# Performance work log

Hardware: AMD Instinct MI355X
Metric: run time of the kernel (lower is better)

## Reference

```python
import jax, jax.numpy as jnp
import numpy as np

N, SD, VD, ED, E, NG, NA, NB = 512, 256, 128, 128, 262144, 16, 16, 5


def _lin_init(key, fan_in, fan_out):
    # torch.nn.Linear default: U(-1/sqrt(fan_in), 1/sqrt(fan_in)); stored as (in, out)
    lim = 1.0 / np.sqrt(fan_in)
    return jax.random.uniform(key, (fan_in, fan_out), jnp.float32, -lim, lim)


def setup_inputs() -> dict:
    key = jax.random.key(0)
    ks = jax.random.split(key, 20)
    s = jax.random.normal(ks[0], (N, SD), jnp.float32)
    v = jax.random.normal(ks[1], (N, 3, VD), jnp.float32)
    p = jax.random.normal(ks[2], (N, 3), jnp.float32)
    e = jax.random.normal(ks[3], (E, ED), jnp.float32)
    batch = jnp.sort(jax.random.randint(ks[4], (N,), 0, NG))
    edge_index_global = jax.random.randint(ks[5], (2, E), 0, N)
    W_sm = _lin_init(ks[6], SD, SD); b_sm = jnp.zeros((SD,), jnp.float32)
    W_bm = _lin_init(ks[7], ED, SD); b_bm = jnp.zeros((SD,), jnp.float32)
    W_b0 = _lin_init(ks[8], SD + 1, SD); b_b0 = jnp.zeros((SD,), jnp.float32)
    W_b1 = _lin_init(ks[9], SD, NB); b_b1 = jnp.zeros((NB,), jnp.float32)
    W_c = _lin_init(ks[10], VD, 1)  # no bias
    W_a = _lin_init(ks[11], SD, NA); b_a = jnp.zeros((NA,), jnp.float32)
    return {"s": s, "v": v, "p": p, "e": e, "batch": batch,
            "edge_index_global": edge_index_global,
            "W_sm": W_sm, "b_sm": b_sm, "W_bm": W_bm, "b_bm": b_bm,
            "W_b0": W_b0, "b_b0": b_b0, "W_b1": W_b1, "b_b1": b_b1,
            "W_c": W_c, "W_a": W_a, "b_a": b_a}


def reference(s, v, p, e, batch, edge_index_global,
              W_sm, b_sm, W_bm, b_bm, W_b0, b_b0, W_b1, b_b1, W_c, W_a, b_a):
    # shared_mapping: Linear + SiLU
    s = jax.nn.silu(s @ W_sm + b_sm)                      # [N, SD]
    coords_pred = (v @ W_c)[..., 0]                       # [N, 3]
    atoms_pred = s @ W_a + b_a                            # [N, NA]
    j, i = edge_index_global[0], edge_index_global[1]
    n = s.shape[0]
    # coords_param == 'data': coords = p + pred, then per-graph mean centering
    coords_pred = p + coords_pred
    seg_sum = jax.ops.segment_sum(coords_pred, batch, num_segments=NG)
    counts = jax.ops.segment_sum(jnp.ones((n, 1), coords_pred.dtype), batch, num_segments=NG)
    mean = seg_sum / jnp.maximum(counts, 1.0)
    coords_pred = coords_pred - mean[batch]
    # squared pairwise distance per edge
    d = jnp.sum((coords_pred[i] - coords_pred[j]) ** 2, axis=-1, keepdims=True)  # [E, 1]
    # sparse -> dense -> sparse symmetrization of edge features (as in the source)
    e_dense = jnp.zeros((n, n, e.shape[-1]), e.dtype).at[j, i].set(e)
    e_dense = 0.5 * (e_dense + jnp.transpose(e_dense, (1, 0, 2)))
    e_sym = e_dense[j, i]                                 # [E, ED]
    f = s[i] + s[j] + (e_sym @ W_bm + b_bm)               # [E, SD]
    edge = jnp.concatenate([f, d], axis=-1)               # [E, SD+1]
    bonds_pred = jax.nn.silu(edge @ W_b0 + b_b0) @ W_b1 + b_b1  # [E, NB]
    return coords_pred, atoms_pred, bonds_pred
```

## Files before the change

### kernel.cpp

```cpp
#include <hip/hip_runtime.h>
#include <math.h>

#define N_NODES 512
#define SD_ 256
#define VD_ 128
#define ED_ 128
#define NE_ 262144
#define NG_ 16
#define NA_ 16
#define NB_ 5
#define MAXP 131328

typedef __attribute__((ext_vector_type(8))) short bf16x8;
typedef __attribute__((ext_vector_type(4))) float f32x4;

__device__ __forceinline__ float silu_f(float x) { return x / (1.0f + expf(-x)); }
__device__ __forceinline__ float silu_fast(float x) {
    return x * __builtin_amdgcn_rcpf(1.0f + __builtin_amdgcn_exp2f(x * -1.44269504f));
}
__device__ __forceinline__ unsigned short f2bf(float x) {
    unsigned int u = __float_as_uint(x);
    return (unsigned short)((u + 0x7fffu + ((u >> 16) & 1u)) >> 16);
}
__device__ __forceinline__ float bf2f(unsigned short h) {
    return __uint_as_float(((unsigned int)h) << 16);
}
__device__ __forceinline__ unsigned int cvt_pk_bf16(float lo, float hi) {
    unsigned int r;
    asm("v_cvt_pk_bf16_f32 %0, %1, %2" : "=v"(r) : "v"(lo), "v"(hi));
    return r;
}

__device__ __forceinline__ void pack_one(
    const float* __restrict__ W, unsigned short* __restrict__ out, int nkb, int idx)
{
    int l = idx & 63;
    int kb = (idx >> 6) % nkb;
    int mtg = idx / (64 * nkb);
    int m = mtg * 16 + (l & 15);
    int k0 = kb * 32 + (l >> 4) * 8;
    bf16x8 pack;
    #pragma unroll
    for (int i = 0; i < 8; ++i) pack[i] = (short)f2bf(W[(size_t)(k0 + i) * SD_ + m]);
    *(bf16x8*)(out + (size_t)idx * 8) = pack;
}

__global__ __launch_bounds__(256) void prep_a(
    const int* __restrict__ ei, int* __restrict__ emap,
    const float* __restrict__ W_bm, const float* __restrict__ W_b0,
    unsigned short* __restrict__ WfA_bm, unsigned short* __restrict__ WfA_b0,
    const float* __restrict__ s, const float* __restrict__ v, const float* __restrict__ p,
    const float* __restrict__ W_sm, const float* __restrict__ b_sm,
    const float* __restrict__ W_a, const float* __restrict__ b_a,
    const float* __restrict__ W_c,
    unsigned short* __restrict__ s2b, float* __restrict__ cpred, float* __restrict__ atoms_out,
    int* __restrict__ counter, float* __restrict__ zrow)
{
    __shared__ float srow[8][SD_];
    __shared__ float s2row[8][SD_];
    const int bid = blockIdx.x;
    const int tid = threadIdx.x;

    if (bid < 1024) {
        int k = bid * 256 + tid;
        int j = ei[k], i = ei[NE_ + k];
        atomicMax(&emap[j * N_NODES + i], k);
        return;
    }
    if (bid < 1072) {
        int idx = (bid - 1024) * 256 + tid;
        if (idx < 4096)  pack_one(W_bm, WfA_bm, 4, idx);
        else             pack_one(W_b0, WfA_b0, 8, idx - 4096);
        return;
    }
    if (bid < 1136) {
        const int n0 = (bid - 1072) * 8;
        #pragma unroll
        for (int n = 0; n < 8; ++n) srow[n][tid] = s[(size_t)(n0 + n) * SD_ + tid];
        __syncthreads();
        float acc[8];
        {
            float bb = b_sm[tid];
            #pragma unroll
            for (int n = 0; n < 8; ++n) acc[n] = bb;
        }
        #pragma unroll 4
        for (int c = 0; c < SD_; ++c) {
            float wv = W_sm[(size_t)c * SD_ + tid];
            #pragma unroll
            for (int n = 0; n < 8; ++n) acc[n] = fmaf(srow[n][c], wv, acc[n]);
        }
        #pragma unroll
        for (int n = 0; n < 8; ++n) {
            float sv = silu_f(acc[n]);
            s2b[(size_t)(n0 + n) * SD_ + tid] = f2bf(sv);
            s2row[n][tid] = sv;
        }
        __syncthreads();
        if (tid < 128) {
            int n = tid >> 4, a = tid & 15;
            float x = b_a[a];
            #pragma unroll 8
            for (int c = 0; c < SD_; ++c) x = fmaf(s2row[n][c], W_a[(size_t)c * NA_ + a], x);
            atoms_out[(size_t)(n0 + n) * NA_ + a] = x;
        }
        return;
    }
    if (tid == 0) counter[0] = 0;
    if (tid < ED_) zrow[tid] = 0.0f;
    for (int o = tid; o < N_NODES * 3; o += 256) {
        float x = p[o];
        const float* vr = v + (size_t)o * VD_;
        #pragma unroll 8
        for (int c = 0; c < VD_; ++c) x = fmaf(vr[c], W_c[c], x);
        cpred[o] = x;
    }
}

__global__ __launch_bounds__(512) void prep_b(
    const float* __restrict__ cpred, const int* __restrict__ batch,
    float* __restrict__ coords_ws, float* __restrict__ coords_out,
    const int* __restrict__ emap, int* __restrict__ counter,
    int* __restrict__ pairslot, int4* __restrict__ worklist)
{
    __shared__ float cl[N_NODES * 3];
    __shared__ int   bl[N_NODES];
    __shared__ float meanv[NG_ * 3];
    const int tid = threadIdx.x;

    if (blockIdx.x == 0) {
        bl[tid] = batch[tid];
        #pragma unroll
        for (int dd = 0; dd < 3; ++dd) cl[tid * 3 + dd] = cpred[tid * 3 + dd];
        __syncthreads();
        if (tid < NG_ * 3) {
            int g = tid / 3, dd = tid % 3;
            float sum = 0.f; int cnt = 0;
            for (int n = 0; n < N_NODES; ++n) {
                if (bl[n] == g) { sum += cl[n * 3 + dd]; cnt++; }
            }
            meanv[tid] = sum / (float)(cnt > 0 ? cnt : 1);
        }
        __syncthreads();
        int g = bl[tid];
        #pragma unroll
        for (int dd = 0; dd < 3; ++dd) {
            float val = cl[tid * 3 + dd] - meanv[g * 3 + dd];
            coords_ws[tid * 3 + dd]  = val;
            coords_out[tid * 3 + dd] = val;
        }
        return;
    }
    int idx = (blockIdx.x - 1) * 512 + tid;
    int a = idx >> 9, b = idx & (N_NODES - 1);
    bool lower = (a <= b);
    int k1 = -1, k2 = -1;
    if (lower) {
        k1 = emap[(a << 9) | b];
        k2 = emap[(b << 9) | a];
    }
    bool qual = lower && (k1 >= 0 || k2 >= 0);
    unsigned long long mask = __ballot(qual);
    if (mask == 0ull) return;
    int lane = tid & 63;
    int leader = __ffsll((unsigned long long)mask) - 1;
    int base = 0;
    if (lane == leader) base = atomicAdd(counter, __popcll(mask));
    base = __shfl(base, leader);
    if (qual) {
        int slot = base + __popcll(mask & ((1ull << lane) - 1ull));
        pairslot[(a << 9) | b] = slot;
        pairslot[(b << 9) | a] = slot;
        worklist[slot] = make_int4(a, b, k1, k2);
    }
}

__global__ __launch_bounds__(256) void bonds_scatter(
    const int* __restrict__ ei, const int* __restrict__ pairslot,
    const float* __restrict__ repval, float* __restrict__ bonds_out)
{
    int k = blockIdx.x * 256 + threadIdx.x;
    int j = ei[k], i = ei[NE_ + k];
    int slot = pairslot[(j << 9) | i];
    const float* rp = repval + (size_t)slot * NB_;
    #pragma unroll
    for (int b = 0; b < NB_; ++b)
        bonds_out[(size_t)k * NB_ + b] = rp[b];
}

__global__ __launch_bounds__(512) void edge_mfma(
    const float* __restrict__ e, const int4* __restrict__ worklist,
    const int* __restrict__ counter, const float* __restrict__ coords,
    const float* __restrict__ zrow, const unsigned short* __restrict__ s2b,
    const unsigned short* __restrict__ WfA_bm, const unsigned short* __restrict__ WfA_b0,
    const float* __restrict__ W_b1,
    const float* __restrict__ b_bm, const float* __restrict__ W_b0_last,
    const float* __restrict__ b_b0, const float* __restrict__ b_b1,
    float* __restrict__ repval)
{
    const int blk = blockIdx.x;
    const int cnt = counter[0];
    if (blk * 64 >= cnt) return;

    __shared__ __align__(16) char smem0[64 * 128 * 2];
    __shared__ __align__(16) unsigned short fd_lds[64 * 256];
    __shared__ unsigned short wb1t[NB_ * 256];
    __shared__ float dw[64];
    __shared__ int li_s[64], lj_s[64];

    unsigned short* esym_lds   = (unsigned short*)smem0;
    float*          bonds_part = (float*)smem0;

    const int tid = threadIdx.x;
    const int l   = tid & 63;
    const int w   = tid >> 6;
    const int eLo = l & 15;
    const int hi  = l >> 4;

    bf16x8 a1pf[4][2];
    #pragma unroll
    for (int kb = 0; kb < 4; ++kb)
        #pragma unroll
        for (int mt = 0; mt < 2; ++mt)
            a1pf[kb][mt] = *(const bf16x8*)(WfA_bm + ((size_t)(((w * 2 + mt) * 4 + kb) * 64 + l) * 8));

    if (tid < 256) {
        const int eL = l;
        const int q  = w;
        int widx = min(blk * 64 + eL, cnt - 1);
        int4 wk = worklist[widx];
        const float* r1 = (wk.z >= 0) ? (e + (size_t)wk.z * ED_) : zrow;
        const float* r2 = (wk.w >= 0) ? (e + (size_t)wk.w * ED_) : zrow;
        const float4* p1 = (const float4*)(r1 + q * 32);
        const float4* p2 = (const float4*)(r2 + q * 32);
        float4 va[8], vb[8];
        #pragma unroll
        for (int t = 0; t < 8; ++t) va[t] = p1[t];
        #pragma unroll
        for (int t = 0; t < 8; ++t) vb[t] = p2[t];
        #pragma unroll
        for (int t = 0; t < 8; ++t) {
            va[t].x += vb[t].x; va[t].y += vb[t].y;
            va[t].z += vb[t].z; va[t].w += vb[t].w;
        }
        int ntB = eL >> 4, eLoB = eL & 15;
        #pragma unroll
        for (int h2 = 0; h2 < 4; ++h2) {
            float4 x0 = va[h2 * 2], x1 = va[h2 * 2 + 1];
            uint4 c;
            c.x = cvt_pk_bf16(0.5f * x0.x, 0.5f * x0.y);
            c.y = cvt_pk_bf16(0.5f * x0.z, 0.5f * x0.w);
            c.z = cvt_pk_bf16(0.5f * x1.x, 0.5f * x1.y);
            c.w = cvt_pk_bf16(0.5f * x1.z, 0.5f * x1.w);
            int chunk = (ntB * 4 + q) * 64 + h2 * 16 + eLoB;
            *(uint4*)(&esym_lds[chunk * 8]) = c;
        }
    } else {
        int t = tid - 256;
        #pragma unroll
        for (int b = 0; b < NB_; ++b)
            wb1t[b * 256 + t] = f2bf(W_b1[(size_t)t * NB_ + b]);
        if (t < 64) {
            int widx = min(blk * 64 + t, cnt - 1);
            int4 wk = worklist[widx];
            li_s[t] = wk.x; lj_s[t] = wk.y;
            float dx = coords[wk.x * 3 + 0] - coords[wk.y * 3 + 0];
            float dy = coords[wk.x * 3 + 1] - coords[wk.y * 3 + 1];
            float dz = coords[wk.x * 3 + 2] - coords[wk.y * 3 + 2];
            dw[t] = dx * dx + dy * dy + dz * dz;
        }
    }

    __syncthreads();

    f32x4 acc[2][4];
    #pragma unroll
    for (int mt = 0; mt < 2; ++mt)
        #pragma unroll
        for (int nt = 0; nt < 4; ++nt) acc[mt][nt] = (f32x4){0.f, 0.f, 0.f, 0.f};

    #pragma unroll
    for (int kb = 0; kb < 4; ++kb) {
        bf16x8 bfg[4];
        #pragma unroll
        for (int nt = 0; nt < 4; ++nt)
            bfg[nt] = *(const bf16x8*)(&esym_lds[(size_t)((nt * 4 + kb) * 64 + l) * 8]);
        __builtin_amdgcn_s_setprio(1);
        #pragma unroll
        for (int mt = 0; mt < 2; ++mt)
            #pragma unroll
            for (int nt = 0; nt < 4; ++nt)
                acc[mt][nt] = __builtin_amdgcn_mfma_f32_16x16x32_bf16(a1pf[kb][mt], bfg[nt], acc[mt][nt], 0, 0, 0);
        __builtin_amdgcn_s_setprio(0);
    }

    bf16x8 a2pf[3][2];
    #pragma unroll
    for (int kb = 0; kb < 3; ++kb)
        #pragma unroll
        for (int mt = 0; mt < 2; ++mt)
            a2pf[kb][mt] = *(const bf16x8*)(WfA_b0 + ((size_t)(((w * 2 + mt) * 8 + kb) * 64 + l) * 8));

    #pragma unroll
    for (int mt = 0; mt < 2; ++mt) {
        int m0 = w * 32 + mt * 16 + hi * 4;
        float4 bb = *(const float4*)(b_bm + m0);
        #pragma unroll
        for (int nt = 0; nt < 4; ++nt) {
            int edge = nt * 16 + eLo;
            int ni = li_s[edge], nj = lj_s[edge];
            ushort4 si = *(const ushort4*)(s2b + (size_t)ni * SD_ + m0);
            ushort4 sj = *(const ushort4*)(s2b + (size_t)nj * SD_ + m0);
            f32x4 r = acc[mt][nt];
            float f0 = r[0] + bf2f(si.x) + bf2f(sj.x) + bb.x;
            float f1 = r[1] + bf2f(si.y) + bf2f(sj.y) + bb.y;
            float f2 = r[2] + bf2f(si.z) + bf2f(sj.z) + bb.z;
            float f3 = r[3] + bf2f(si.w) + bf2f(sj.w) + bb.w;
            uint2 pk;
            pk.x = cvt_pk_bf16(f0, f1);
            pk.y = cvt_pk_bf16(f2, f3);
            int c16 = m0 >> 3;
            int byteo = (edge << 9) + ((c16 ^ (edge & 7)) << 4) + ((m0 & 7) << 1);
            *(uint2*)((char*)fd_lds + byteo) = pk;
        }
    }
    __syncthreads();

    #pragma unroll
    for (int mt = 0; mt < 2; ++mt) {
        int m0 = w * 32 + mt * 16 + hi * 4;
        float4 b0 = *(const float4*)(b_b0 + m0);
        float4 w2 = *(const float4*)(W_b0_last + m0);
        #pragma unroll
        for (int nt = 0; nt < 4; ++nt) {
            float dd = dw[nt * 16 + eLo];
            acc[mt][nt] = (f32x4){fmaf(dd, w2.x, b0.x), fmaf(dd, w2.y, b0.y),
                                  fmaf(dd, w2.z, b0.z), fmaf(dd, w2.w, b0.w)};
        }
    }
    #pragma unroll
    for (int kb = 0; kb < 8; ++kb) {
        bf16x8 af[2], bfg[4];
        #pragma unroll
        for (int mt = 0; mt < 2; ++mt)
            af[mt] = (kb < 3) ? a2pf[kb][mt]
                   : *(const bf16x8*)(WfA_b0 + ((size_t)(((w * 2 + mt) * 8 + kb) * 64 + l) * 8));
        #pragma unroll
        for (int nt = 0; nt < 4; ++nt) {
            int edge = nt * 16 + eLo;
            int c16 = (kb << 2) + hi;
            int byteo = (edge << 9) + ((c16 ^ (edge & 7)) << 4);
            bfg[nt] = *(const bf16x8*)((const char*)fd_lds + byteo);
        }
        __builtin_amdgcn_s_setprio(1);
        #pragma unroll
        for (int mt = 0; mt < 2; ++mt)
            #pragma unroll
            for (int nt = 0; nt < 4; ++nt)
                acc[mt][nt] = __builtin_amdgcn_mfma_f32_16x16x32_bf16(af[mt], bfg[nt], acc[mt][nt], 0, 0, 0);
        __builtin_amdgcn_s_setprio(0);
    }

    float pb[4][NB_];
    #pragma unroll
    for (int nt = 0; nt < 4; ++nt)
        #pragma unroll
        for (int b = 0; b < NB_; ++b) pb[nt][b] = 0.f;
    #pragma unroll
    for (int mt = 0; mt < 2; ++mt) {
        int m0 = w * 32 + mt * 16 + hi * 4;
        ushort4 wv[NB_];
        #pragma unroll
        for (int b = 0; b < NB_; ++b)
            wv[b] = *(const ushort4*)(wb1t + b * 256 + m0);
        #pragma unroll
        for (int nt = 0; nt < 4; ++nt) {
            f32x4 r = acc[mt][nt];
            float h0 = silu_fast(r[0]);
            float h1 = silu_fast(r[1]);
            float h2 = silu_fast(r[2]);
            float h3 = silu_fast(r[3]);
            #pragma unroll
            for (int b = 0; b < NB_; ++b) {
                float t = fmaf(h0, bf2f(wv[b].x), fmaf(h1, bf2f(wv[b].y),
                          fmaf(h2, bf2f(wv[b].z), h3 * bf2f(wv[b].w))));
                pb[nt][b] += t;
            }
        }
    }
    #pragma unroll
    for (int off = 16; off <= 32; off <<= 1)
        #pragma unroll
        for (int nt = 0; nt < 4; ++nt)
            #pragma unroll
            for (int b = 0; b < NB_; ++b)
                pb[nt][b] += __shfl_xor(pb[nt][b], off);

    __syncthreads();
    if (hi == 0) {
        #pragma unroll
        for (int nt = 0; nt < 4; ++nt)
            #pragma unroll
            for (int b = 0; b < NB_; ++b)
                bonds_part[(size_t)(w * 64 + nt * 16 + eLo) * NB_ + b] = pb[nt][b];
    }
    __syncthreads();

    for (int idx = tid; idx < 64 * NB_; idx += 512) {
        int edge = idx / NB_, b = idx % NB_;
        float s8 = 0.f;
        #pragma unroll
        for (int pp = 0; pp < 8; ++pp)
            s8 += bonds_part[(size_t)(pp * 64 + edge) * NB_ + b];
        repval[(size_t)(blk * 64 + edge) * NB_ + b] = s8 + b_b1[b];
    }
}

extern "C" void kernel_launch(void* const* d_in, const int* in_sizes, int n_in,
                              void* d_out, int out_size, void* d_ws, size_t ws_size,
                              hipStream_t stream)
{
    const float* s    = (const float*)d_in[0];
    const float* v    = (const float*)d_in[1];
    const float* p    = (const float*)d_in[2];
    const float* e    = (const float*)d_in[3];
    const int*   batch= (const int*)d_in[4];
    const int*   ei   = (const int*)d_in[5];
    const float* W_sm = (const float*)d_in[6];
    const float* b_sm = (const float*)d_in[7];
    const float* W_bm = (const float*)d_in[8];
    const float* b_bm = (const float*)d_in[9];
    const float* W_b0 = (const float*)d_in[10];
    const float* b_b0 = (const float*)d_in[11];
    const float* W_b1 = (const float*)d_in[12];
    const float* b_b1 = (const float*)d_in[13];
    const float* W_c  = (const float*)d_in[14];
    const float* W_a  = (const float*)d_in[15];
    const float* b_a  = (const float*)d_in[16];

    float* out = (float*)d_out;
    float* coords_out = out;
    float* atoms_out  = out + 1536;
    float* bonds_out  = out + 1536 + 8192;

    char* ws = (char*)d_ws;
    int*            emap    = (int*)ws;
    unsigned short* s2b     = (unsigned short*)(ws + 0x100000);
    unsigned short* WfA_bm  = (unsigned short*)(ws + 0x140000);
    unsigned short* WfA_b0  = (unsigned short*)(ws + 0x150000);
    float*          cpred   = (float*)(ws + 0x170000);
    float*          coords  = (float*)(ws + 0x172000);
    int*            counter = (int*)(ws + 0x175000);
    float*          zrow    = (float*)(ws + 0x175100);
    int*            pairslot= (int*)(ws + 0x180000);
    int4*           worklist= (int4*)(ws + 0x280000);
    float*          repval  = (float*)(ws + 0x4B0000);

    prep_a<<<1137, 256, 0, stream>>>(ei, emap, W_bm, W_b0, WfA_bm, WfA_b0,
                                     s, v, p, W_sm, b_sm, W_a, b_a, W_c,
                                     s2b, cpred, atoms_out, counter, zrow);
    prep_b<<<513, 512, 0, stream>>>(cpred, batch, coords, coords_out,
                                    emap, counter, pairslot, worklist);

    edge_mfma<<<(MAXP + 63) / 64, 512, 0, stream>>>(e, worklist, counter, coords, zrow, s2b,
                                                    WfA_bm, WfA_b0, W_b1,
                                                    b_bm, W_b0 + 256 * SD_, b_b0, b_b1,
                                                    repval);
    bonds_scatter<<<NE_ / 256, 256, 0, stream>>>(ei, pairslot, repval, bonds_out);
}
```

Measured before the change: 142.8 us.

## Fold W_bm into W_b0 and precompute per-node S·W_b0 to drop second GEMM

Because no nonlinearity sits between the bond-message linear and the first bond MLP layer, the two weight matrices are pre-multiplied into one fused 128x256 matrix. The node terms s[i]+s[j] are precomputed per node as s·W_b0 and gathered, and the biases are folded into a single vector. Each edge block then runs one K=128 MFMA GEMM instead of a K=128 plus a K=256 GEMM, and processes two 64-pair tiles per block. The cost is extra prep work (weight product, per-node projection) and a change in rounding, since the fused weight is rounded to bf16 once while the intermediate f was previously rounded too.

```diff
diff --git a/kernel.cpp b/kernel.cpp
--- a/kernel.cpp
+++ b/kernel.cpp
@@ -31,30 +31,17 @@
     return r;
 }
 
-__device__ __forceinline__ void pack_one(
-    const float* __restrict__ W, unsigned short* __restrict__ out, int nkb, int idx)
-{
-    int l = idx & 63;
-    int kb = (idx >> 6) % nkb;
-    int mtg = idx / (64 * nkb);
-    int m = mtg * 16 + (l & 15);
-    int k0 = kb * 32 + (l >> 4) * 8;
-    bf16x8 pack;
-    #pragma unroll
-    for (int i = 0; i < 8; ++i) pack[i] = (short)f2bf(W[(size_t)(k0 + i) * SD_ + m]);
-    *(bf16x8*)(out + (size_t)idx * 8) = pack;
-}
-
 __global__ __launch_bounds__(256) void prep_a(
     const int* __restrict__ ei, int* __restrict__ emap,
     const float* __restrict__ W_bm, const float* __restrict__ W_b0,
-    unsigned short* __restrict__ WfA_bm, unsigned short* __restrict__ WfA_b0,
+    unsigned short* __restrict__ WfF,
     const float* __restrict__ s, const float* __restrict__ v, const float* __restrict__ p,
     const float* __restrict__ W_sm, const float* __restrict__ b_sm,
     const float* __restrict__ W_a, const float* __restrict__ b_a,
     const float* __restrict__ W_c,
-    unsigned short* __restrict__ s2b, float* __restrict__ cpred, float* __restrict__ atoms_out,
-    int* __restrict__ counter, float* __restrict__ zrow)
+    const float* __restrict__ b_bm, const float* __restrict__ b_b0,
+    float* __restrict__ s2f, float* __restrict__ cpred, float* __restrict__ atoms_out,
+    int* __restrict__ counter, float* __restrict__ zrow, float* __restrict__ bias2)
 {
     __shared__ float srow[8][SD_];
     __shared__ float s2row[8][SD_];
@@ -67,14 +54,30 @@
         atomicMax(&emap[j * N_NODES + i], k);
         return;
     }
-    if (bid < 1072) {
-        int idx = (bid - 1024) * 256 + tid;
-        if (idx < 4096)  pack_one(W_bm, WfA_bm, 4, idx);
-        else             pack_one(W_b0, WfA_b0, 8, idx - 4096);
-        return;
-    }
-    if (bid < 1136) {
-        const int n0 = (bid - 1072) * 8;
+    if (bid < 1040) {
+        int mtg = bid - 1024;
+        int kb = tid >> 6;
+        int l  = tid & 63;
+        int m  = mtg * 16 + (l & 15);
+        int k0 = kb * 32 + (l >> 4) * 8;
+        float a8[8];
+        #pragma unroll
+        for (int i = 0; i < 8; ++i) a8[i] = 0.f;
+        for (int c = 0; c < SD_; ++c) {
+            float wb0 = W_b0[(size_t)c * SD_ + m];
+            #pragma unroll
+            for (int i = 0; i < 8; ++i)
+                a8[i] = fmaf(W_bm[(size_t)(k0 + i) * SD_ + c], wb0, a8[i]);
+        }
+        bf16x8 pack;
+        #pragma unroll
+        for (int i = 0; i < 8; ++i) pack[i] = (short)f2bf(a8[i]);
+        int idx = (mtg * 4 + kb) * 64 + l;
+        *(bf16x8*)(WfF + (size_t)idx * 8) = pack;
+        return;
+    }
+    if (bid < 1104) {
+        const int n0 = (bid - 1040) * 8;
         #pragma unroll
         for (int n = 0; n < 8; ++n) srow[n][tid] = s[(size_t)(n0 + n) * SD_ + tid];
         __syncthreads();
@@ -93,7 +96,7 @@
         #pragma unroll
         for (int n = 0; n < 8; ++n) {
             float sv = silu_f(acc[n]);
-            s2b[(size_t)(n0 + n) * SD_ + tid] = f2bf(sv);
+            s2f[(size_t)(n0 + n) * SD_ + tid] = sv;
             s2row[n][tid] = sv;
         }
         __syncthreads();
@@ -106,14 +109,23 @@
         }
         return;
     }
-    if (tid == 0) counter[0] = 0;
-    if (tid < ED_) zrow[tid] = 0.0f;
-    for (int o = tid; o < N_NODES * 3; o += 256) {
-        float x = p[o];
-        const float* vr = v + (size_t)o * VD_;
-        #pragma unroll 8
-        for (int c = 0; c < VD_; ++c) x = fmaf(vr[c], W_c[c], x);
-        cpred[o] = x;
+    if (bid == 1104) {
+        if (tid == 0) counter[0] = 0;
+        if (tid < ED_) zrow[tid] = 0.0f;
+        for (int o = tid; o < N_NODES * 3; o += 256) {
+            float x = p[o];
+            const float* vr = v + (size_t)o * VD_;
+            #pragma unroll 8
+            for (int c = 0; c < VD_; ++c) x = fmaf(vr[c], W_c[c], x);
+            cpred[o] = x;
+        }
+        return;
+    }
+    {
+        float acc = b_b0[tid];
+        for (int c = 0; c < SD_; ++c)
+            acc = fmaf(b_bm[c], W_b0[(size_t)c * SD_ + tid], acc);
+        bias2[tid] = acc;
     }
 }
 
@@ -121,14 +133,17 @@
     const float* __restrict__ cpred, const int* __restrict__ batch,
     float* __restrict__ coords_ws, float* __restrict__ coords_out,
     const int* __restrict__ emap, int* __restrict__ counter,
-    int* __restrict__ pairslot, int4* __restrict__ worklist)
+    int* __restrict__ pairslot, int4* __restrict__ worklist,
+    const float* __restrict__ s2f, const float* __restrict__ W_b0,
+    float* __restrict__ S2W)
 {
     __shared__ float cl[N_NODES * 3];
     __shared__ int   bl[N_NODES];
     __shared__ float meanv[NG_ * 3];
     const int tid = threadIdx.x;
-
-    if (blockIdx.x == 0) {
+    const int bid = blockIdx.x;
+
+    if (bid == 0) {
         bl[tid] = batch[tid];
         #pragma unroll
         for (int dd = 0; dd < 3; ++dd) cl[tid * 3 + dd] = cpred[tid * 3 + dd];
@@ -151,27 +166,45 @@
         }
         return;
     }
-    int idx = (blockIdx.x - 1) * 512 + tid;
-    int a = idx >> 9, b = idx & (N_NODES - 1);
-    bool lower = (a <= b);
-    int k1 = -1, k2 = -1;
-    if (lower) {
-        k1 = emap[(a << 9) | b];
-        k2 = emap[(b << 9) | a];
-    }
-    bool qual = lower && (k1 >= 0 || k2 >= 0);
-    unsigned long long mask = __ballot(qual);
-    if (mask == 0ull) return;
-    int lane = tid & 63;
-    int leader = __ffsll((unsigned long long)mask) - 1;
-    int base = 0;
-    if (lane == leader) base = atomicAdd(counter, __popcll(mask));
-    base = __shfl(base, leader);
-    if (qual) {
-        int slot = base + __popcll(mask & ((1ull << lane) - 1ull));
-        pairslot[(a << 9) | b] = slot;
-        pairslot[(b << 9) | a] = slot;
-        worklist[slot] = make_int4(a, b, k1, k2);
+    if (bid <= 512) {
+        int idx = (bid - 1) * 512 + tid;
+        int a = idx >> 9, b = idx & (N_NODES - 1);
+        bool lower = (a <= b);
+        int k1 = -1, k2 = -1;
+        if (lower) {
+            k1 = emap[(a << 9) | b];
+            k2 = emap[(b << 9) | a];
+        }
+        bool qual = lower && (k1 >= 0 || k2 >= 0);
+        unsigned long long mask = __ballot(qual);
+        if (mask == 0ull) return;
+        int lane = tid & 63;
+        int leader = __ffsll((unsigned long long)mask) - 1;
+        int base = 0;
+        if (lane == leader) base = atomicAdd(counter, __popcll(mask));
+        base = __shfl(base, leader);
+        if (qual) {
+            int slot = base + __popcll(mask & ((1ull << lane) - 1ull));
+            pairslot[(a << 9) | b] = slot;
+            pairslot[(b << 9) | a] = slot;
+            worklist[slot] = make_int4(a, b, k1, k2);
+        }
+        return;
+    }
+    {
+        __shared__ float srows[2][SD_];
+        int n0 = (bid - 513) * 2;
+        if (tid < 512) {
+            int n = tid >> 8, c = tid & 255;
+            srows[n][c] = s2f[(size_t)(n0 + n) * SD_ + c];
+        }
+        __syncthreads();
+        int n = tid >> 8, m = tid & 255;
+        float acc = 0.f;
+        #pragma unroll 8
+        for (int c = 0; c < SD_; ++c)
+            acc = fmaf(srows[n][c], W_b0[(size_t)c * SD_ + m], acc);
+        S2W[(size_t)(n0 + n) * SD_ + m] = acc;
     }
 }
 
@@ -191,25 +224,22 @@
 __global__ __launch_bounds__(512) void edge_mfma(
     const float* __restrict__ e, const int4* __restrict__ worklist,
     const int* __restrict__ counter, const float* __restrict__ coords,
-    const float* __restrict__ zrow, const unsigned short* __restrict__ s2b,
-    const unsigned short* __restrict__ WfA_bm, const unsigned short* __restrict__ WfA_b0,
-    const float* __restrict__ W_b1,
-    const float* __restrict__ b_bm, const float* __restrict__ W_b0_last,
-    const float* __restrict__ b_b0, const float* __restrict__ b_b1,
+    const float* __restrict__ zrow,
+    const unsigned short* __restrict__ WfF, const float* __restrict__ S2W,
+    const float* __restrict__ bias2,
+    const float* __restrict__ W_b1, const float* __restrict__ W_b0_last,
+    const float* __restrict__ b_b1,
     float* __restrict__ repval)
 {
     const int blk = blockIdx.x;
     const int cnt = counter[0];
-    if (blk * 64 >= cnt) return;
-
-    __shared__ __align__(16) char smem0[64 * 128 * 2];
-    __shared__ __align__(16) unsigned short fd_lds[64 * 256];
+    if (blk * 128 >= cnt) return;
+
+    __shared__ __align__(16) unsigned short esym_lds[2][64 * 128];
     __shared__ unsigned short wb1t[NB_ * 256];
-    __shared__ float dw[64];
-    __shared__ int li_s[64], lj_s[64];
-
-    unsigned short* esym_lds   = (unsigned short*)smem0;
-    float*          bonds_part = (float*)smem0;
+    __shared__ float bonds_part[8 * 64 * NB_];
+    __shared__ float dw[128];
+    __shared__ int li_s[128], lj_s[128];
 
     const int tid = threadIdx.x;
     const int l   = tid & 63;
@@ -222,12 +252,13 @@
     for (int kb = 0; kb < 4; ++kb)
         #pragma unroll
         for (int mt = 0; mt < 2; ++mt)
-            a1pf[kb][mt] = *(const bf16x8*)(WfA_bm + ((size_t)(((w * 2 + mt) * 4 + kb) * 64 + l) * 8));
-
-    if (tid < 256) {
-        const int eL = l;
-        const int q  = w;
-        int widx = min(blk * 64 + eL, cnt - 1);
+            a1pf[kb][mt] = *(const bf16x8*)(WfF + ((size_t)(((w * 2 + mt) * 4 + kb) * 64 + l) * 8));
+
+    {
+        const int tile = w >> 2;
+        const int q    = w & 3;
+        const int eL   = l;
+        int widx = min(blk * 128 + tile * 64 + eL, cnt - 1);
         int4 wk = worklist[widx];
         const float* r1 = (wk.z >= 0) ? (e + (size_t)wk.z * ED_) : zrow;
         const float* r2 = (wk.w >= 0) ? (e + (size_t)wk.w * ED_) : zrow;
@@ -253,166 +284,120 @@
             c.z = cvt_pk_bf16(0.5f * x1.x, 0.5f * x1.y);
             c.w = cvt_pk_bf16(0.5f * x1.z, 0.5f * x1.w);
             int chunk = (ntB * 4 + q) * 64 + h2 * 16 + eLoB;
-            *(uint4*)(&esym_lds[chunk * 8]) = c;
-        }
-    } else {
-        int t = tid - 256;
+            *(uint4*)(&esym_lds[tile][chunk * 8]) = c;
+        }
+    }
+
+    if (tid < 128) {
+        int widx = min(blk * 128 + tid, cnt - 1);
+        int4 wk = worklist[widx];
+        li_s[tid] = wk.x; lj_s[tid] = wk.y;
+        float dx = coords[wk.x * 3 + 0] - coords[wk.y * 3 + 0];
+        float dy = coords[wk.x * 3 + 1] - coords[wk.y * 3 + 1];
+        float dz = coords[wk.x * 3 + 2] - coords[wk.y * 3 + 2];
+        dw[tid] = dx * dx + dy * dy + dz * dz;
+    }
+    if (tid < 256) {
         #pragma unroll
         for (int b = 0; b < NB_; ++b)
-            wb1t[b * 256 + t] = f2bf(W_b1[(size_t)t * NB_ + b]);
-        if (t < 64) {
-            int widx = min(blk * 64 + t, cnt - 1);
-            int4 wk = worklist[widx];
-            li_s[t] = wk.x; lj_s[t] = wk.y;
-            float dx = coords[wk.x * 3 + 0] - coords[wk.y * 3 + 0];
-            float dy = coords[wk.x * 3 + 1] - coords[wk.y * 3 + 1];
-            float dz = coords[wk.x * 3 + 2] - coords[wk.y * 3 + 2];
-            dw[t] = dx * dx + dy * dy + dz * dz;
-        }
+            wb1t[b * 256 + tid] = f2bf(W_b1[(size_t)tid * NB_ + b]);
     }
 
     __syncthreads();
 
     f32x4 acc[2][4];
+    float pb[4][NB_];
+
     #pragma unroll
-    for (int mt = 0; mt < 2; ++mt)
-        #pragma unroll
-        for (int nt = 0; nt < 4; ++nt) acc[mt][nt] = (f32x4){0.f, 0.f, 0.f, 0.f};
-
-    #pragma unroll
-    for (int kb = 0; kb < 4; ++kb) {
-        bf16x8 bfg[4];
+    for (int tile = 0; tile < 2; ++tile) {
+        const int pbase = tile * 64;
+
+        #pragma unroll
+        for (int mt = 0; mt < 2; ++mt) {
+            int m0 = w * 32 + mt * 16 + hi * 4;
+            float4 bz = *(const float4*)(bias2 + m0);
+            float4 w2 = *(const float4*)(W_b0_last + m0);
+            #pragma unroll
+            for (int nt = 0; nt < 4; ++nt) {
+                int pair = pbase + nt * 16 + eLo;
+                int na = li_s[pair], nb2 = lj_s[pair];
+                float4 sa  = *(const float4*)(S2W + (size_t)na  * SD_ + m0);
+                float4 sb4 = *(const float4*)(S2W + (size_t)nb2 * SD_ + m0);
+                float dd = dw[pair];
+                acc[mt][nt] = (f32x4){fmaf(dd, w2.x, bz.x) + sa.x + sb4.x,
+                                      fmaf(dd, w2.y, bz.y) + sa.y + sb4.y,
+                                      fmaf(dd, w2.z, bz.z) + sa.z + sb4.z,
+                                      fmaf(dd, w2.w, bz.w) + sa.w + sb4.w};
+            }
+        }
+
+        #pragma unroll
+        for (int kb = 0; kb < 4; ++kb) {
+            bf16x8 bfg[4];
+            #pragma unroll
+            for (int nt = 0; nt < 4; ++nt)
+                bfg[nt] = *(const bf16x8*)(&esym_lds[tile][(size_t)((nt * 4 + kb) * 64 + l) * 8]);
+            __builtin_amdgcn_s_setprio(1);
+            #pragma unroll
+            for (int mt = 0; mt < 2; ++mt)
+                #pragma unroll
+                for (int nt = 0; nt < 4; ++nt)
+                    acc[mt][nt] = __builtin_amdgcn_mfma_f32_16x16x32_bf16(a1pf[kb][mt], bfg[nt], acc[mt][nt], 0, 0, 0);
+            __builtin_amdgcn_s_setprio(0);
+        }
+
         #pragma unroll
         for (int nt = 0; nt < 4; ++nt)
-            bfg[nt] = *(const bf16x8*)(&esym_lds[(size_t)((nt * 4 + kb) * 64 + l) * 8]);
-        __builtin_amdgcn_s_setprio(1);
-        #pragma unroll
-        for (int mt = 0; mt < 2; ++mt)
+            #pragma unroll
+            for (int b = 0; b < NB_; ++b) pb[nt][b] = 0.f;
+        #pragma unroll
+        for (int mt = 0; mt < 2; ++mt) {
+            int m0 = w * 32 + mt * 16 + hi * 4;
+            ushort4 wv[NB_];
+            #pragma unroll
+            for (int b = 0; b < NB_; ++b)
+                wv[b] = *(const ushort4*)(wb1t + b * 256 + m0);
+            #pragma unroll
+            for (int nt = 0; nt < 4; ++nt) {
+                f32x4 r = acc[mt][nt];
+                float h0 = silu_fast(r[0]);
+                float h1 = silu_fast(r[1]);
+                float h2 = silu_fast(r[2]);
+                float h3 = silu_fast(r[3]);
+                #pragma unroll
+                for (int b = 0; b < NB_; ++b) {
+                    float t = fmaf(h0, bf2f(wv[b].x), fmaf(h1, bf2f(wv[b].y),
+                              fmaf(h2, bf2f(wv[b].z), h3 * bf2f(wv[b].w))));
+                    pb[nt][b] += t;
+                }
+            }
+        }
+        #pragma unroll
+        for (int off = 16; off <= 32; off <<= 1)
             #pragma unroll
             for (int nt = 0; nt < 4; ++nt)
-                acc[mt][nt] = __builtin_amdgcn_mfma_f32_16x16x32_bf16(a1pf[kb][mt], bfg[nt], acc[mt][nt], 0, 0, 0);
-        __builtin_amdgcn_s_setprio(0);
-    }
-
-    bf16x8 a2pf[3][2];
-    #pragma unroll
-    for (int kb = 0; kb < 3; ++kb)
-        #pragma unroll
-        for (int mt = 0; mt < 2; ++mt)
-            a2pf[kb][mt] = *(const bf16x8*)(WfA_b0 + ((size_t)(((w * 2 + mt) * 8 + kb) * 64 + l) * 8));
-
-    #pragma unroll
-    for (int mt = 0; mt < 2; ++mt) {
-        int m0 = w * 32 + mt * 16 + hi * 4;
-        float4 bb = *(const float4*)(b_bm + m0);
-        #pragma unroll
-        for (int nt = 0; nt < 4; ++nt) {
-            int edge = nt * 16 + eLo;
-            int ni = li_s[edge], nj = lj_s[edge];
-            ushort4 si = *(const ushort4*)(s2b + (size_t)ni * SD_ + m0);
-            ushort4 sj = *(const ushort4*)(s2b + (size_t)nj * SD_ + m0);
-            f32x4 r = acc[mt][nt];
-            float f0 = r[0] + bf2f(si.x) + bf2f(sj.x) + bb.x;
-            float f1 = r[1] + bf2f(si.y) + bf2f(sj.y) + bb.y;
-            float f2 = r[2] + bf2f(si.z) + bf2f(sj.z) + bb.z;
-            float f3 = r[3] + bf2f(si.w) + bf2f(sj.w) + bb.w;
-            uint2 pk;
-            pk.x = cvt_pk_bf16(f0, f1);
-            pk.y = cvt_pk_bf16(f2, f3);
-            int c16 = m0 >> 3;
-            int byteo = (edge << 9) + ((c16 ^ (edge & 7)) << 4) + ((m0 & 7) << 1);
-            *(uint2*)((char*)fd_lds + byteo) = pk;
-        }
-    }
-    __syncthreads();
-
-    #pragma unroll
-    for (int mt = 0; mt < 2; ++mt) {
-        int m0 = w * 32 + mt * 16 + hi * 4;
-        float4 b0 = *(const float4*)(b_b0 + m0);
-        float4 w2 = *(const float4*)(W_b0_last + m0);
-        #pragma unroll
-        for (int nt = 0; nt < 4; ++nt) {
-            float dd = dw[nt * 16 + eLo];
-            acc[mt][nt] = (f32x4){fmaf(dd, w2.x, b0.x), fmaf(dd, w2.y, b0.y),
-                                  fmaf(dd, w2.z, b0.z), fmaf(dd, w2.w, b0.w)};
-        }
-    }
-    #pragma unroll
-    for (int kb = 0; kb < 8; ++kb) {
-        bf16x8 af[2], bfg[4];
-        #pragma unroll
-        for (int mt = 0; mt < 2; ++mt)
-            af[mt] = (kb < 3) ? a2pf[kb][mt]
-                   : *(const bf16x8*)(WfA_b0 + ((size_t)(((w * 2 + mt) * 8 + kb) * 64 + l) * 8));
-        #pragma unroll
-        for (int nt = 0; nt < 4; ++nt) {
-            int edge = nt * 16 + eLo;
-            int c16 = (kb << 2) + hi;
-            int byteo = (edge << 9) + ((c16 ^ (edge & 7)) << 4);
-            bfg[nt] = *(const bf16x8*)((const char*)fd_lds + byteo);
-        }
-        __builtin_amdgcn_s_setprio(1);
-        #pragma unroll
-        for (int mt = 0; mt < 2; ++mt)
+                #pragma unroll
+                for (int b = 0; b < NB_; ++b)
+                    pb[nt][b] += __shfl_xor(pb[nt][b], off);
+
+        if (tile == 1) __syncthreads();
+        if (hi == 0) {
             #pragma unroll
             for (int nt = 0; nt < 4; ++nt)
-                acc[mt][nt] = __builtin_amdgcn_mfma_f32_16x16x32_bf16(af[mt], bfg[nt], acc[mt][nt], 0, 0, 0);
-        __builtin_amdgcn_s_setprio(0);
-    }
-
-    float pb[4][NB_];
-    #pragma unroll
-    for (int nt = 0; nt < 4; ++nt)
-        #pragma unroll
-        for (int b = 0; b < NB_; ++b) pb[nt][b] = 0.f;
-    #pragma unroll
-    for (int mt = 0; mt < 2; ++mt) {
-        int m0 = w * 32 + mt * 16 + hi * 4;
-        ushort4 wv[NB_];
-        #pragma unroll
-        for (int b = 0; b < NB_; ++b)
-            wv[b] = *(const ushort4*)(wb1t + b * 256 + m0);
-        #pragma unroll
-        for (int nt = 0; nt < 4; ++nt) {
-            f32x4 r = acc[mt][nt];
-            float h0 = silu_fast(r[0]);
-            float h1 = silu_fast(r[1]);
-            float h2 = silu_fast(r[2]);
-            float h3 = silu_fast(r[3]);
-            #pragma unroll
-            for (int b = 0; b < NB_; ++b) {
-                float t = fmaf(h0, bf2f(wv[b].x), fmaf(h1, bf2f(wv[b].y),
-                          fmaf(h2, bf2f(wv[b].z), h3 * bf2f(wv[b].w))));
-                pb[nt][b] += t;
-            }
-        }
-    }
-    #pragma unroll
-    for (int off = 16; off <= 32; off <<= 1)
-        #pragma unroll
-        for (int nt = 0; nt < 4; ++nt)
-            #pragma unroll
-            for (int b = 0; b < NB_; ++b)
-                pb[nt][b] += __shfl_xor(pb[nt][b], off);
-
-    __syncthreads();
-    if (hi == 0) {
-        #pragma unroll
-        for (int nt = 0; nt < 4; ++nt)
-            #pragma unroll
-            for (int b = 0; b < NB_; ++b)
-                bonds_part[(size_t)(w * 64 + nt * 16 + eLo) * NB_ + b] = pb[nt][b];
-    }
-    __syncthreads();
-
-    for (int idx = tid; idx < 64 * NB_; idx += 512) {
-        int edge = idx / NB_, b = idx % NB_;
-        float s8 = 0.f;
-        #pragma unroll
-        for (int pp = 0; pp < 8; ++pp)
-            s8 += bonds_part[(size_t)(pp * 64 + edge) * NB_ + b];
-        repval[(size_t)(blk * 64 + edge) * NB_ + b] = s8 + b_b1[b];
+                #pragma unroll
+                for (int b = 0; b < NB_; ++b)
+                    bonds_part[(size_t)(w * 64 + nt * 16 + eLo) * NB_ + b] = pb[nt][b];
+        }
+        __syncthreads();
+
+        for (int idx = tid; idx < 64 * NB_; idx += 512) {
+            int edge = idx / NB_, b = idx % NB_;
+            float s8 = 0.f;
+            #pragma unroll
+            for (int pp = 0; pp < 8; ++pp)
+                s8 += bonds_part[(size_t)(pp * 64 + edge) * NB_ + b];
+            repval[(size_t)(blk * 128 + pbase + edge) * NB_ + b] = s8 + b_b1[b];
+        }
     }
 }
 
@@ -445,26 +430,29 @@
 
     char* ws = (char*)d_ws;
     int*            emap    = (int*)ws;
-    unsigned short* s2b     = (unsigned short*)(ws + 0x100000);
-    unsigned short* WfA_bm  = (unsigned short*)(ws + 0x140000);
-    unsigned short* WfA_b0  = (unsigned short*)(ws + 0x150000);
-    float*          cpred   = (float*)(ws + 0x170000);
-    float*          coords  = (float*)(ws + 0x172000);
-    int*            counter = (int*)(ws + 0x175000);
-    float*          zrow    = (float*)(ws + 0x175100);
-    int*            pairslot= (int*)(ws + 0x180000);
-    int4*           worklist= (int4*)(ws + 0x280000);
-    float*          repval  = (float*)(ws + 0x4B0000);
-
-    prep_a<<<1137, 256, 0, stream>>>(ei, emap, W_bm, W_b0, WfA_bm, WfA_b0,
+    float*          s2f     = (float*)(ws + 0x100000);
+    unsigned short* WfF     = (unsigned short*)(ws + 0x180000);
+    float*          S2W     = (float*)(ws + 0x190000);
+    float*          bias2   = (float*)(ws + 0x210000);
+    float*          cpred   = (float*)(ws + 0x211000);
+    float*          coords  = (float*)(ws + 0x213000);
+    int*            counter = (int*)(ws + 0x215000);
+    float*          zrow    = (float*)(ws + 0x215100);
+    int*            pairslot= (int*)(ws + 0x2A0000);
+    int4*           worklist= (int4*)(ws + 0x3A0000);
+    float*          repval  = (float*)(ws + 0x5D0000);
+
+    prep_a<<<1106, 256, 0, stream>>>(ei, emap, W_bm, W_b0, WfF,
                                      s, v, p, W_sm, b_sm, W_a, b_a, W_c,
-                                     s2b, cpred, atoms_out, counter, zrow);
-    prep_b<<<513, 512, 0, stream>>>(cpred, batch, coords, coords_out,
-                                    emap, counter, pairslot, worklist);
-
-    edge_mfma<<<(MAXP + 63) / 64, 512, 0, stream>>>(e, worklist, counter, coords, zrow, s2b,
-                                                    WfA_bm, WfA_b0, W_b1,
-                                                    b_bm, W_b0 + 256 * SD_, b_b0, b_b1,
-                                                    repval);
+                                     b_bm, b_b0,
+                                     s2f, cpred, atoms_out, counter, zrow, bias2);
+    prep_b<<<769, 512, 0, stream>>>(cpred, batch, coords, coords_out,
+                                    emap, counter, pairslot, worklist,
+                                    s2f, W_b0, S2W);
+
+    edge_mfma<<<(MAXP + 127) / 128, 512, 0, stream>>>(e, worklist, counter, coords, zrow,
+                                                      WfF, S2W, bias2,
+                                                      W_b1, W_b0 + 256 * SD_, b_b1,
+                                                      repval);
     bonds_scatter<<<NE_ / 256, 256, 0, stream>>>(ei, pairslot, repval, bonds_out);
 }
```

Result: slower. 150.1 us (+5.1%).
